# Optimization experiments

Measured on AMD Instinct MI355X. Metric: run time of the kernel, lower is better.

Reference implementation:

```python
import jax, jax.numpy as jnp
import numpy as np

NUM_HEADS = 16
EPS = 1e-5


def _layernorm(x, w):
    # torch LayerNorm (biased variance), bias=False
    m = jnp.mean(x, axis=-1, keepdims=True)
    v = jnp.mean(jnp.square(x - m), axis=-1, keepdims=True)
    return (x - m) * jax.lax.rsqrt(v + EPS) * w


def setup_inputs() -> dict:
    key = jax.random.key(0)
    ks = jax.random.split(key, 8)
    B, S, H, A = 2, 2048, 1024, 1024
    hd = H // NUM_HEADS
    return {
        "x": jax.random.normal(ks[0], (B, S, H), jnp.float32),
        "ada_cond": jax.random.normal(ks[1], (B, A), jnp.float32),
        "freqs": jax.random.normal(ks[2], (S, hd // 2, 2), jnp.float32),
        "w_qkv": jax.random.normal(ks[3], (3 * H, H), jnp.float32) * (1.0 / np.sqrt(H)),
        "w_o": jax.random.normal(ks[4], (H, H), jnp.float32) * (1.0 / np.sqrt(H)),
        "ln_w": jnp.ones((H,), jnp.float32),
        "mod_w": jax.random.normal(ks[5], (3 * H, A), jnp.float32) * 0.02,
        "mod_b": jax.random.normal(ks[6], (3 * H,), jnp.float32) * 0.02,
        "qn_w": jnp.ones((hd,), jnp.float32),
        "kn_w": jnp.ones((hd,), jnp.float32),
    }


def reference(x, ada_cond, freqs, w_qkv, w_o, ln_w, mod_w, mod_b, qn_w, kn_w):
    B, S, H = x.shape
    nh = NUM_HEADS
    hd = H // nh

    # pre-norm + AdaLN modulation (with gate)
    h = _layernorm(x, ln_w)
    mod = (jax.nn.silu(ada_cond) @ mod_w.T + mod_b)[:, None, :]  # [B,1,3H]
    scale, shift, gate = jnp.split(mod, 3, axis=-1)
    h = h * (scale + 1.0) + shift

    # QKV projection and head split
    qkv = h @ w_qkv.T                                  # [B,S,3H]
    q, k, v = jnp.split(qkv, 3, axis=-1)
    to_heads = lambda t: t.reshape(B, S, nh, hd).transpose(0, 2, 1, 3)  # [B,nh,S,hd]
    q, k, v = to_heads(q), to_heads(k), to_heads(v)

    # per-head QK layernorm
    q = _layernorm(q, qn_w)
    k = _layernorm(k, kn_w)

    # RoPE (complex rotation via interleaved pairs)
    f = freqs[:S].reshape(1, 1, S, hd // 2, 2)

    def rope(t):
        tr = t.reshape(B, nh, S, hd // 2, 2)
        re = tr[..., 0] * f[..., 0] - tr[..., 1] * f[..., 1]
        im = tr[..., 1] * f[..., 0] + tr[..., 0] * f[..., 1]
        return jnp.stack([re, im], axis=-1).reshape(B, nh, S, hd)

    q, k = rope(q), rope(k)

    # scaled dot-product attention (non-causal)
    scores = jnp.einsum("bhqd,bhkd->bhqk", q, k) * (1.0 / np.sqrt(hd))
    attn = jax.nn.softmax(scores, axis=-1)
    o = jnp.einsum("bhqk,bhkd->bhqd", attn, v)
    o = o.transpose(0, 2, 1, 3).reshape(B, S, H)

    return (o @ w_o.T) * gate
```

## Files before the change

kernel.cpp:

```cpp
#include <hip/hip_runtime.h>
#include <hip/hip_bf16.h>
#include <hip/hip_fp16.h>
#include <math.h>

#define B_ 2
#define S_ 2048
#define H_ 1024
#define A_ 1024
#define NH_ 16
#define HD_ 64
#define H3_ 3072
#define EPS_ 1e-5f

typedef __attribute__((ext_vector_type(8))) short short8;
typedef __attribute__((ext_vector_type(4))) float floatx4;
typedef __attribute__((ext_vector_type(4))) _Float16 half4v;
typedef __attribute__((ext_vector_type(2))) __fp16 fp16x2;

__device__ inline unsigned short f2bf(float x) {
    union { float f; unsigned u; } v; v.f = x;
    unsigned r = v.u + 0x7fffu + ((v.u >> 16) & 1u);
    return (unsigned short)(r >> 16);
}

__device__ inline unsigned pk_bf16(float a, float b) {
    union { __hip_bfloat162 h; unsigned u; } v;
    v.h = __float22bfloat162_rn(make_float2(a, b));
    return v.u;
}

__device__ inline unsigned pk_f16(float a, float b) {
    union { __half2 h; unsigned u; } v;
    v.h = __float22half2_rn(make_float2(a, b));
    return v.u;
}

__device__ inline void gld_lds16(const void* g, void* l) {
    __builtin_amdgcn_global_load_lds(
        (const __attribute__((address_space(1))) unsigned int*)g,
        (__attribute__((address_space(3))) unsigned int*)l, 16, 0, 0);
}


__global__ __launch_bounds__(256) void cast_bf16_kernel(
    const float* __restrict__ in, unsigned short* __restrict__ out, int n)
{
    int i = (blockIdx.x * 256 + threadIdx.x) * 8;
    if (i >= n) return;
    float4 a = *(const float4*)(in + i);
    float4 b = *(const float4*)(in + i + 4);
    uint4 o;
    o.x = pk_bf16(a.x, a.y);
    o.y = pk_bf16(a.z, a.w);
    o.z = pk_bf16(b.x, b.y);
    o.w = pk_bf16(b.z, b.w);
    *(uint4*)(out + i) = o;
}

__global__ __launch_bounds__(256) void mod_gemv_kernel(
    const float* __restrict__ ada, const float* __restrict__ mod_w,
    const float* __restrict__ mod_b, float* __restrict__ mod)
{
    int wid = threadIdx.x >> 6;
    int lane = threadIdx.x & 63;
    int idx = blockIdx.x * 4 + wid;
    int b = idx / H3_;
    int j = idx % H3_;
    const float* ar = ada + (size_t)b * A_;
    const float* wr = mod_w + (size_t)j * A_;
    float acc = 0.f;
    for (int a = lane; a < A_; a += 64) {
        float av = ar[a];
        float sv = av / (1.f + __expf(-av));
        acc += sv * wr[a];
    }
    #pragma unroll
    for (int m = 1; m < 64; m <<= 1) acc += __shfl_xor(acc, m);
    if (lane == 0) mod[idx] = acc + mod_b[j];
}

__global__ __launch_bounds__(256) void ln_mod_kernel(
    const float* __restrict__ x, const float* __restrict__ ln_w,
    const float* __restrict__ mod, unsigned short* __restrict__ hout)
{
    int row = blockIdx.x;
    int b = row >> 11;
    const float* xr = x + (size_t)row * H_;
    int t = threadIdx.x;
    float4 xv = *(const float4*)(xr + t * 4);
    float s1 = xv.x + xv.y + xv.z + xv.w;
    float s2 = xv.x*xv.x + xv.y*xv.y + xv.z*xv.z + xv.w*xv.w;
    #pragma unroll
    for (int m = 1; m < 64; m <<= 1) { s1 += __shfl_xor(s1, m); s2 += __shfl_xor(s2, m); }
    __shared__ float r1[4], r2[4];
    int wid = t >> 6, lane = t & 63;
    if (lane == 0) { r1[wid] = s1; r2[wid] = s2; }
    __syncthreads();
    s1 = r1[0] + r1[1] + r1[2] + r1[3];
    s2 = r2[0] + r2[1] + r2[2] + r2[3];
    float mean = s1 * (1.f / H_);
    float var  = s2 * (1.f / H_) - mean * mean;
    float rstd = rsqrtf(var + EPS_);
    const float* mrow = mod + (size_t)b * H3_;
    float4 wv = *(const float4*)(ln_w + t * 4);
    float4 sc = *(const float4*)(mrow + t * 4);
    float4 sh = *(const float4*)(mrow + H_ + t * 4);
    float4 hv;
    hv.x = (xv.x - mean) * rstd * wv.x * (sc.x + 1.f) + sh.x;
    hv.y = (xv.y - mean) * rstd * wv.y * (sc.y + 1.f) + sh.y;
    hv.z = (xv.z - mean) * rstd * wv.z * (sc.z + 1.f) + sh.z;
    hv.w = (xv.w - mean) * rstd * wv.w * (sc.w + 1.f) + sh.w;
    uint2 o;
    o.x = pk_bf16(hv.x, hv.y);
    o.y = pk_bf16(hv.z, hv.w);
    *(uint2*)(hout + (size_t)row * H_ + t * 4) = o;
}

__global__ __launch_bounds__(256) void gemm_qkv_fused_kernel(
    const unsigned short* __restrict__ A, const unsigned short* __restrict__ Bm,
    const float* __restrict__ freqs, const float* __restrict__ qn_w,
    const float* __restrict__ kn_w, unsigned short* __restrict__ qout,
    unsigned short* __restrict__ kout, unsigned short* __restrict__ vtout)
{
    __shared__ unsigned short As[2][128 * 32];
    __shared__ unsigned short Bs[2][128 * 32];
    const int K = H_;
    int t = threadIdx.x;
    int w = t >> 6, lane = t & 63;
    int q16 = lane & 15, quad = lane >> 4;
    int wm = w >> 1, wn = w & 1;
    int m0 = blockIdx.y * 128, n0 = blockIdx.x * 128;

    int srow = 2 * (lane >> 3) + ((lane >> 2) & 1);
    int scol = ((lane & 3) ^ ((lane >> 3) & 3)) << 3;
    const unsigned short* ga = A + (size_t)(m0 + (w << 5) + srow) * K + scol;
    const unsigned short* gb = Bm + (size_t)(n0 + (w << 5) + srow) * K + scol;
    int ldst0 = (w * 16) * 64;
    int ldst1 = (w * 16 + 8) * 64;

    floatx4 acc[4][4];
    #pragma unroll
    for (int mt = 0; mt < 4; ++mt)
        #pragma unroll
        for (int nt = 0; nt < 4; ++nt)
            acc[mt][nt] = (floatx4){0.f, 0.f, 0.f, 0.f};

    int abase = (wm * 32 + (q16 >> 1)) * 64 + (q16 & 1) * 32
              + ((quad ^ ((q16 >> 1) & 3)) << 3);
    int bbase = (wn * 32 + (q16 >> 1)) * 64 + (q16 & 1) * 32
              + ((quad ^ ((q16 >> 1) & 3)) << 3);

    gld_lds16(ga, &As[0][ldst0]);
    gld_lds16(ga + (size_t)16 * K, &As[0][ldst1]);
    gld_lds16(gb, &Bs[0][ldst0]);
    gld_lds16(gb + (size_t)16 * K, &Bs[0][ldst1]);
    __syncthreads();

    int cur = 0;
    for (int kt = 0; kt < K / 32; ++kt) {
        const unsigned short* curA = &As[cur][0];
        const unsigned short* curB = &Bs[cur][0];
        short8 af[4], bf[4];
        #pragma unroll
        for (int mt = 0; mt < 4; ++mt)
            af[mt] = *(const short8*)&curA[abase + mt * 512];
        #pragma unroll
        for (int nt = 0; nt < 4; ++nt)
            bf[nt] = *(const short8*)&curB[bbase + nt * 512];

        if (kt + 1 < K / 32) {
            const unsigned short* ga2 = ga + (kt + 1) * 32;
            const unsigned short* gb2 = gb + (kt + 1) * 32;
            int nb = cur ^ 1;
            gld_lds16(ga2, &As[nb][ldst0]);
            gld_lds16(ga2 + (size_t)16 * K, &As[nb][ldst1]);
            gld_lds16(gb2, &Bs[nb][ldst0]);
            gld_lds16(gb2 + (size_t)16 * K, &Bs[nb][ldst1]);
        }

        #pragma unroll
        for (int mt = 0; mt < 4; ++mt)
            #pragma unroll
            for (int nt = 0; nt < 4; ++nt)
                acc[mt][nt] = __builtin_amdgcn_mfma_f32_16x16x32_bf16(
                    af[mt], bf[nt], acc[mt][nt], 0, 0, 0);

        __syncthreads();
        cur ^= 1;
    }

    int n_base = n0 + wn * 64;
    int sec = n_base >> 10;
    int head = (n_base & 1023) >> 6;

    if (sec == 2) {
        #pragma unroll
        for (int mt = 0; mt < 4; ++mt) {
            int m = m0 + wm * 64 + mt * 16 + quad * 4;
            int b = m >> 11, s = m & (S_ - 1);
            #pragma unroll
            for (int nt = 0; nt < 4; ++nt) {
                int d = nt * 16 + q16;
                unsigned short* dst =
                    vtout + ((size_t)((b * 16 + head) * 64 + d)) * S_ + s;
                uint2 pk;
                pk.x = pk_f16(acc[mt][nt][0], acc[mt][nt][1]);
                pk.y = pk_f16(acc[mt][nt][2], acc[mt][nt][3]);
                *(uint2*)dst = pk;
            }
        }
    } else {
        const float* nw = (sec == 0) ? qn_w : kn_w;
        float w4[4];
        #pragma unroll
        for (int nt = 0; nt < 4; ++nt) w4[nt] = nw[nt * 16 + q16];
        unsigned short* outp = (sec == 0) ? qout : kout;
        float qscale = (sec == 0) ? 0.1803368801111244f : 1.0f;

        #pragma unroll
        for (int mt = 0; mt < 4; ++mt) {
            #pragma unroll
            for (int i = 0; i < 4; ++i) {
                int m = m0 + wm * 64 + mt * 16 + quad * 4 + i;
                int b = m >> 11, s = m & (S_ - 1);
                float v0 = acc[mt][0][i], v1 = acc[mt][1][i];
                float v2 = acc[mt][2][i], v3 = acc[mt][3][i];
                float s1 = (v0 + v1) + (v2 + v3);
                float s2 = (v0 * v0 + v1 * v1) + (v2 * v2 + v3 * v3);
                #pragma unroll
                for (int msk = 1; msk < 16; msk <<= 1) {
                    s1 += __shfl_xor(s1, msk);
                    s2 += __shfl_xor(s2, msk);
                }
                float mean = s1 * (1.f / 64);
                float var  = s2 * (1.f / 64) - mean * mean;
                float rstd = rsqrtf(var + EPS_);
                float vv[4];
                vv[0] = (v0 - mean) * rstd * w4[0];
                vv[1] = (v1 - mean) * rstd * w4[1];
                vv[2] = (v2 - mean) * rstd * w4[2];
                vv[3] = (v3 - mean) * rstd * w4[3];
                const float* fr = freqs + (size_t)s * 64;
                unsigned short* orow = outp + ((size_t)((b * 16 + head) * S_ + s)) * 64;
                #pragma unroll
                for (int nt = 0; nt < 4; ++nt) {
                    int c = nt * 16 + q16;
                    float vp = __shfl_xor(vv[nt], 1);
                    float2 ff = *(const float2*)(fr + (c & ~1));
                    float r = (c & 1) ? (vv[nt] * ff.x + vp * ff.y)
                                      : (vv[nt] * ff.x - vp * ff.y);
                    orow[c] = f2bf(r * qscale);
                }
            }
        }
    }
}

__global__ __launch_bounds__(256) void gemm_bt_bf16_kernel(
    const unsigned short* __restrict__ A, const unsigned short* __restrict__ Bm,
    float* __restrict__ C, int M, int N, int K,
    const float* __restrict__ gate, int gate_stride, int batch_shift)
{
    __shared__ unsigned short As[2][128 * 32];
    __shared__ unsigned short Bs[2][128 * 32];
    int t = threadIdx.x;
    int w = t >> 6, lane = t & 63;
    int q16 = lane & 15, quad = lane >> 4;
    int wm = w >> 1, wn = w & 1;
    int m0 = blockIdx.y * 128, n0 = blockIdx.x * 128;

    int srow = 2 * (lane >> 3) + ((lane >> 2) & 1);
    int scol = ((lane & 3) ^ ((lane >> 3) & 3)) << 3;
    const unsigned short* ga = A + (size_t)(m0 + (w << 5) + srow) * K + scol;
    const unsigned short* gb = Bm + (size_t)(n0 + (w << 5) + srow) * K + scol;
    int ldst0 = (w * 16) * 64;
    int ldst1 = (w * 16 + 8) * 64;

    floatx4 acc[4][4];
    #pragma unroll
    for (int mt = 0; mt < 4; ++mt)
        #pragma unroll
        for (int nt = 0; nt < 4; ++nt)
            acc[mt][nt] = (floatx4){0.f, 0.f, 0.f, 0.f};

    int abase = (wm * 32 + (q16 >> 1)) * 64 + (q16 & 1) * 32
              + ((quad ^ ((q16 >> 1) & 3)) << 3);
    int bbase = (wn * 32 + (q16 >> 1)) * 64 + (q16 & 1) * 32
              + ((quad ^ ((q16 >> 1) & 3)) << 3);

    gld_lds16(ga, &As[0][ldst0]);
    gld_lds16(ga + (size_t)16 * K, &As[0][ldst1]);
    gld_lds16(gb, &Bs[0][ldst0]);
    gld_lds16(gb + (size_t)16 * K, &Bs[0][ldst1]);
    __syncthreads();

    int cur = 0;
    for (int kt = 0; kt < K / 32; ++kt) {
        const unsigned short* curA = &As[cur][0];
        const unsigned short* curB = &Bs[cur][0];
        short8 af[4], bf[4];
        #pragma unroll
        for (int mt = 0; mt < 4; ++mt)
            af[mt] = *(const short8*)&curA[abase + mt * 512];
        #pragma unroll
        for (int nt = 0; nt < 4; ++nt)
            bf[nt] = *(const short8*)&curB[bbase + nt * 512];

        if (kt + 1 < K / 32) {
            const unsigned short* ga2 = ga + (kt + 1) * 32;
            const unsigned short* gb2 = gb + (kt + 1) * 32;
            int nb = cur ^ 1;
            gld_lds16(ga2, &As[nb][ldst0]);
            gld_lds16(ga2 + (size_t)16 * K, &As[nb][ldst1]);
            gld_lds16(gb2, &Bs[nb][ldst0]);
            gld_lds16(gb2 + (size_t)16 * K, &Bs[nb][ldst1]);
        }

        #pragma unroll
        for (int mt = 0; mt < 4; ++mt)
            #pragma unroll
            for (int nt = 0; nt < 4; ++nt)
                acc[mt][nt] = __builtin_amdgcn_mfma_f32_16x16x32_bf16(
                    af[mt], bf[nt], acc[mt][nt], 0, 0, 0);

        __syncthreads();
        cur ^= 1;
    }

    #pragma unroll
    for (int mt = 0; mt < 4; ++mt) {
        #pragma unroll
        for (int i = 0; i < 4; ++i) {
            int m = m0 + wm * 64 + mt * 16 + quad * 4 + i;
            float* crow = C + (size_t)m * N;
            const float* grow = gate ? gate + (size_t)(m >> batch_shift) * gate_stride
                                     : nullptr;
            #pragma unroll
            for (int nt = 0; nt < 4; ++nt) {
                int n = n0 + wn * 64 + nt * 16 + q16;
                float v = acc[mt][nt][i];
                if (gate) v *= grow[n];
                crow[n] = v;
            }
        }
    }
}

__global__ __launch_bounds__(256, 2) void attn_mfma_kernel(
    const unsigned short* __restrict__ q, const unsigned short* __restrict__ k,
    const unsigned short* __restrict__ vt, unsigned short* __restrict__ o)
{
    __shared__ __align__(16) unsigned char smem[16 * 1024];
    __shared__ float lbuf[4][4][16];
    unsigned short* Vs = (unsigned short*)smem;

    int t = threadIdx.x;
    int w = t >> 6, lane = t & 63;
    int q16 = lane & 15, quad = lane >> 4;
    int bh = blockIdx.y, b = bh >> 4, h = bh & 15;
    int s0 = blockIdx.x * 64;

    const unsigned short* qgp = q + ((size_t)bh * S_ + s0) * HD_;
    short8 qf[4][2];
    #pragma unroll
    for (int qg = 0; qg < 4; ++qg)
        #pragma unroll
        for (int hh = 0; hh < 2; ++hh)
            qf[qg][hh] = *(const short8*)(qgp + (16 * qg + q16) * HD_ + hh * 32 + quad * 8);

    const unsigned short* kg = k + (size_t)bh * S_ * HD_ + (16 * w + q16) * HD_ + quad * 8;

    const unsigned short* vg0 = vt + (size_t)bh * 64 * S_
                              + (size_t)(16 * w + (lane >> 3)) * S_ + (lane & 7) * 8;
    const unsigned short* vg1 = vg0 + 8 * S_;
    unsigned short* vw0 = Vs + (16 * w + (lane >> 3)) * 64 + (((lane & 7) ^ (lane >> 3)) << 3);
    unsigned short* vw1 = vw0 + 512;
    int vroff = q16 * 64 + (((2 * w + (quad >> 1)) ^ (q16 & 7)) << 3) + ((quad & 1) << 2);

    short8 kf_nx0 = *(const short8*)kg;
    short8 kf_nx1 = *(const short8*)(kg + 32);
    uint4 vr0 = *(const uint4*)vg0;
    uint4 vr1 = *(const uint4*)vg1;

    union { half4v h; uint2 u; } ones;
    ones.u.x = 0x3C003C00u; ones.u.y = 0x3C003C00u;

    floatx4 acc_o[4][4];
    floatx4 acc_l[4];
    #pragma unroll
    for (int nd = 0; nd < 4; ++nd)
        #pragma unroll
        for (int qg = 0; qg < 4; ++qg)
            acc_o[nd][qg] = (floatx4){0.f, 0.f, 0.f, 0.f};
    #pragma unroll
    for (int qg = 0; qg < 4; ++qg) acc_l[qg] = (floatx4){0.f, 0.f, 0.f, 0.f};

    for (int kt = 0; kt < S_ / 64; ++kt) {
        short8 kf0 = kf_nx0, kf1 = kf_nx1;
        uint4 v0 = vr0, v1 = vr1;
        __syncthreads();
        *(uint4*)vw0 = v0;
        *(uint4*)vw1 = v1;
        __syncthreads();

        if (kt + 1 < S_ / 64) {
            kg += 64 * HD_; vg0 += 64; vg1 += 64;
            kf_nx0 = *(const short8*)kg;
            kf_nx1 = *(const short8*)(kg + 32);
            vr0 = *(const uint4*)vg0;
            vr1 = *(const uint4*)vg1;
        }

        floatx4 sc[4];
        #pragma unroll
        for (int qg = 0; qg < 4; ++qg) sc[qg] = (floatx4){-12.f, -12.f, -12.f, -12.f};
        #pragma unroll
        for (int qg = 0; qg < 4; ++qg) {
            sc[qg] = __builtin_amdgcn_mfma_f32_16x16x32_bf16(kf0, qf[qg][0], sc[qg], 0, 0, 0);
            sc[qg] = __builtin_amdgcn_mfma_f32_16x16x32_bf16(kf1, qf[qg][1], sc[qg], 0, 0, 0);
        }

        half4v vf[4];
        #pragma unroll
        for (int nd = 0; nd < 4; ++nd)
            vf[nd] = *(const half4v*)&Vs[vroff + nd * 1024];

        #pragma unroll
        for (int qg = 0; qg < 4; ++qg) {
            float p0 = __builtin_amdgcn_exp2f(sc[qg][0]);
            float p1 = __builtin_amdgcn_exp2f(sc[qg][1]);
            float p2 = __builtin_amdgcn_exp2f(sc[qg][2]);
            float p3 = __builtin_amdgcn_exp2f(sc[qg][3]);
            union { half4v h; fp16x2 f2[2]; } pf;
            pf.f2[0] = __builtin_amdgcn_cvt_pkrtz(p0, p1);
            pf.f2[1] = __builtin_amdgcn_cvt_pkrtz(p2, p3);
            acc_l[qg] = __builtin_amdgcn_mfma_f32_16x16x16f16(ones.h, pf.h, acc_l[qg], 0, 0, 0);
            #pragma unroll
            for (int nd = 0; nd < 4; ++nd)
                acc_o[nd][qg] = __builtin_amdgcn_mfma_f32_16x16x16f16(
                    vf[nd], pf.h, acc_o[nd][qg], 0, 0, 0);
        }
    }

    if (quad == 0) {
        #pragma unroll
        for (int qg = 0; qg < 4; ++qg) lbuf[w][qg][q16] = acc_l[qg][0];
    }
    __syncthreads();
    float linv = 1.f / (lbuf[0][w][q16] + lbuf[1][w][q16] + lbuf[2][w][q16] + lbuf[3][w][q16]);

    float* obuf = (float*)smem;
    float* myw = obuf + ((w * 4) * 64 + lane) * 4;
    float* myr = obuf + (w * 64 + lane) * 4;
    unsigned short* og = o + ((size_t)(b * S_ + s0 + 16 * w + q16)) * H_ + h * HD_ + 4 * quad;

    #pragma unroll
    for (int nd = 0; nd < 4; ++nd) {
        __syncthreads();
        #pragma unroll
        for (int qg = 0; qg < 4; ++qg)
            *(floatx4*)(myw + qg * 256) = acc_o[nd][qg];
        __syncthreads();
        floatx4 r0 = *(const floatx4*)(myr);
        floatx4 r1 = *(const floatx4*)(myr + 1024);
        floatx4 r2 = *(const floatx4*)(myr + 2048);
        floatx4 r3 = *(const floatx4*)(myr + 3072);
        floatx4 s = (r0 + r1) + (r2 + r3);
        uint2 pk;
        pk.x = pk_bf16(s[0] * linv, s[1] * linv);
        pk.y = pk_bf16(s[2] * linv, s[3] * linv);
        *(uint2*)(og + nd * 16) = pk;
    }
}

extern "C" void kernel_launch(void* const* d_in, const int* in_sizes, int n_in,
                              void* d_out, int out_size, void* d_ws, size_t ws_size,
                              hipStream_t stream)
{
    const float* x     = (const float*)d_in[0];
    const float* ada   = (const float*)d_in[1];
    const float* freqs = (const float*)d_in[2];
    const float* w_qkv = (const float*)d_in[3];
    const float* w_o   = (const float*)d_in[4];
    const float* ln_w  = (const float*)d_in[5];
    const float* mod_w = (const float*)d_in[6];
    const float* mod_b = (const float*)d_in[7];
    const float* qn_w  = (const float*)d_in[8];
    const float* kn_w  = (const float*)d_in[9];
    float* out = (float*)d_out;

    float* ws  = (float*)d_ws;
    float* mod = ws;
    unsigned short* hb    = (unsigned short*)(mod + 8192);
    unsigned short* qb    = hb + (size_t)B_ * S_ * H_;
    unsigned short* kb    = qb + (size_t)B_ * S_ * H_;
    unsigned short* vtb   = kb + (size_t)B_ * S_ * H_;
    unsigned short* ob    = vtb + (size_t)B_ * S_ * H_;
    unsigned short* wqkvb = ob + (size_t)B_ * S_ * H_;
    unsigned short* wob   = wqkvb + (size_t)H3_ * H_;

    cast_bf16_kernel<<<H3_ * H_ / (8 * 256), 256, 0, stream>>>(w_qkv, wqkvb, H3_ * H_);
    cast_bf16_kernel<<<H_ * H_ / (8 * 256), 256, 0, stream>>>(w_o, wob, H_ * H_);
    mod_gemv_kernel<<<B_ * H3_ / 4, 256, 0, stream>>>(ada, mod_w, mod_b, mod);
    ln_mod_kernel<<<B_ * S_, 256, 0, stream>>>(x, ln_w, mod, hb);
    gemm_qkv_fused_kernel<<<dim3(H3_ / 128, B_ * S_ / 128), 256, 0, stream>>>(
        hb, wqkvb, freqs, qn_w, kn_w, qb, kb, vtb);
    attn_mfma_kernel<<<dim3(S_ / 64, B_ * NH_), 256, 0, stream>>>(qb, kb, vtb, ob);
    gemm_bt_bf16_kernel<<<dim3(H_ / 128, B_ * S_ / 128), 256, 0, stream>>>(
        ob, wob, out, B_ * S_, H_, H_, mod + 2 * H_, H3_, 11);
}
```

Measured before the change: 263.6 us.

## Load V fragments directly from global in attention; shrink output GEMM tile to 128x64

The attention kernel stops staging V through LDS with two barriers per key tile. Each lane now loads its V fragments straight from global memory into registers and prefetches the next tile's fragments. This removes the per-iteration syncthreads and LDS traffic, at the cost of smaller, less coalesced global reads and more registers. The output-projection GEMM also moves from 128x128 to 128x64 tiles, doubling the block count from 256 to 512 to fill more CUs, but with less operand reuse per block.

```diff
diff --git a/kernel.cpp b/kernel.cpp
--- a/kernel.cpp
+++ b/kernel.cpp
@@ -262,45 +262,44 @@
     const float* __restrict__ gate, int gate_stride, int batch_shift)
 {
     __shared__ unsigned short As[2][128 * 32];
-    __shared__ unsigned short Bs[2][128 * 32];
+    __shared__ unsigned short Bs[2][64 * 32];
     int t = threadIdx.x;
     int w = t >> 6, lane = t & 63;
     int q16 = lane & 15, quad = lane >> 4;
-    int wm = w >> 1, wn = w & 1;
-    int m0 = blockIdx.y * 128, n0 = blockIdx.x * 128;
+    int m0 = blockIdx.y * 128, n0 = blockIdx.x * 64;
 
     int srow = 2 * (lane >> 3) + ((lane >> 2) & 1);
     int scol = ((lane & 3) ^ ((lane >> 3) & 3)) << 3;
     const unsigned short* ga = A + (size_t)(m0 + (w << 5) + srow) * K + scol;
-    const unsigned short* gb = Bm + (size_t)(n0 + (w << 5) + srow) * K + scol;
-    int ldst0 = (w * 16) * 64;
-    int ldst1 = (w * 16 + 8) * 64;
-
-    floatx4 acc[4][4];
-    #pragma unroll
-    for (int mt = 0; mt < 4; ++mt)
+    const unsigned short* gb = Bm + (size_t)(n0 + (w << 4) + srow) * K + scol;
+    int ldstA0 = (w * 16) * 64;
+    int ldstA1 = (w * 16 + 8) * 64;
+    int ldstB  = (w * 8) * 64;
+
+    floatx4 acc[2][4];
+    #pragma unroll
+    for (int mt = 0; mt < 2; ++mt)
         #pragma unroll
         for (int nt = 0; nt < 4; ++nt)
             acc[mt][nt] = (floatx4){0.f, 0.f, 0.f, 0.f};
 
-    int abase = (wm * 32 + (q16 >> 1)) * 64 + (q16 & 1) * 32
+    int abase = (w * 16 + (q16 >> 1)) * 64 + (q16 & 1) * 32
               + ((quad ^ ((q16 >> 1) & 3)) << 3);
-    int bbase = (wn * 32 + (q16 >> 1)) * 64 + (q16 & 1) * 32
+    int bbase = (q16 >> 1) * 64 + (q16 & 1) * 32
               + ((quad ^ ((q16 >> 1) & 3)) << 3);
 
-    gld_lds16(ga, &As[0][ldst0]);
-    gld_lds16(ga + (size_t)16 * K, &As[0][ldst1]);
-    gld_lds16(gb, &Bs[0][ldst0]);
-    gld_lds16(gb + (size_t)16 * K, &Bs[0][ldst1]);
+    gld_lds16(ga, &As[0][ldstA0]);
+    gld_lds16(ga + (size_t)16 * K, &As[0][ldstA1]);
+    gld_lds16(gb, &Bs[0][ldstB]);
     __syncthreads();
 
     int cur = 0;
     for (int kt = 0; kt < K / 32; ++kt) {
         const unsigned short* curA = &As[cur][0];
         const unsigned short* curB = &Bs[cur][0];
-        short8 af[4], bf[4];
-        #pragma unroll
-        for (int mt = 0; mt < 4; ++mt)
+        short8 af[2], bf[4];
+        #pragma unroll
+        for (int mt = 0; mt < 2; ++mt)
             af[mt] = *(const short8*)&curA[abase + mt * 512];
         #pragma unroll
         for (int nt = 0; nt < 4; ++nt)
@@ -310,14 +309,13 @@
             const unsigned short* ga2 = ga + (kt + 1) * 32;
             const unsigned short* gb2 = gb + (kt + 1) * 32;
             int nb = cur ^ 1;
-            gld_lds16(ga2, &As[nb][ldst0]);
-            gld_lds16(ga2 + (size_t)16 * K, &As[nb][ldst1]);
-            gld_lds16(gb2, &Bs[nb][ldst0]);
-            gld_lds16(gb2 + (size_t)16 * K, &Bs[nb][ldst1]);
-        }
-
-        #pragma unroll
-        for (int mt = 0; mt < 4; ++mt)
+            gld_lds16(ga2, &As[nb][ldstA0]);
+            gld_lds16(ga2 + (size_t)16 * K, &As[nb][ldstA1]);
+            gld_lds16(gb2, &Bs[nb][ldstB]);
+        }
+
+        #pragma unroll
+        for (int mt = 0; mt < 2; ++mt)
             #pragma unroll
             for (int nt = 0; nt < 4; ++nt)
                 acc[mt][nt] = __builtin_amdgcn_mfma_f32_16x16x32_bf16(
@@ -328,16 +326,16 @@
     }
 
     #pragma unroll
-    for (int mt = 0; mt < 4; ++mt) {
+    for (int mt = 0; mt < 2; ++mt) {
         #pragma unroll
         for (int i = 0; i < 4; ++i) {
-            int m = m0 + wm * 64 + mt * 16 + quad * 4 + i;
+            int m = m0 + w * 32 + mt * 16 + quad * 4 + i;
             float* crow = C + (size_t)m * N;
             const float* grow = gate ? gate + (size_t)(m >> batch_shift) * gate_stride
                                      : nullptr;
             #pragma unroll
             for (int nt = 0; nt < 4; ++nt) {
-                int n = n0 + wn * 64 + nt * 16 + q16;
+                int n = n0 + nt * 16 + q16;
                 float v = acc[mt][nt][i];
                 if (gate) v *= grow[n];
                 crow[n] = v;
@@ -350,9 +348,8 @@
     const unsigned short* __restrict__ q, const unsigned short* __restrict__ k,
     const unsigned short* __restrict__ vt, unsigned short* __restrict__ o)
 {
-    __shared__ __align__(16) unsigned char smem[16 * 1024];
+    __shared__ __align__(16) float obuf[4096];
     __shared__ float lbuf[4][4][16];
-    unsigned short* Vs = (unsigned short*)smem;
 
     int t = threadIdx.x;
     int w = t >> 6, lane = t & 63;
@@ -369,18 +366,15 @@
             qf[qg][hh] = *(const short8*)(qgp + (16 * qg + q16) * HD_ + hh * 32 + quad * 8);
 
     const unsigned short* kg = k + (size_t)bh * S_ * HD_ + (16 * w + q16) * HD_ + quad * 8;
-
-    const unsigned short* vg0 = vt + (size_t)bh * 64 * S_
-                              + (size_t)(16 * w + (lane >> 3)) * S_ + (lane & 7) * 8;
-    const unsigned short* vg1 = vg0 + 8 * S_;
-    unsigned short* vw0 = Vs + (16 * w + (lane >> 3)) * 64 + (((lane & 7) ^ (lane >> 3)) << 3);
-    unsigned short* vw1 = vw0 + 512;
-    int vroff = q16 * 64 + (((2 * w + (quad >> 1)) ^ (q16 & 7)) << 3) + ((quad & 1) << 2);
+    const unsigned short* vg = vt + (size_t)bh * 64 * S_ + (size_t)q16 * S_
+                             + 16 * w + quad * 4;
 
     short8 kf_nx0 = *(const short8*)kg;
     short8 kf_nx1 = *(const short8*)(kg + 32);
-    uint4 vr0 = *(const uint4*)vg0;
-    uint4 vr1 = *(const uint4*)vg1;
+    half4v vf_nx[4];
+    #pragma unroll
+    for (int nd = 0; nd < 4; ++nd)
+        vf_nx[nd] = *(const half4v*)(vg + nd * 16 * S_);
 
     union { half4v h; uint2 u; } ones;
     ones.u.x = 0x3C003C00u; ones.u.y = 0x3C003C00u;
@@ -397,18 +391,15 @@
 
     for (int kt = 0; kt < S_ / 64; ++kt) {
         short8 kf0 = kf_nx0, kf1 = kf_nx1;
-        uint4 v0 = vr0, v1 = vr1;
-        __syncthreads();
-        *(uint4*)vw0 = v0;
-        *(uint4*)vw1 = v1;
-        __syncthreads();
+        half4v vf0 = vf_nx[0], vf1 = vf_nx[1], vf2 = vf_nx[2], vf3 = vf_nx[3];
 
         if (kt + 1 < S_ / 64) {
-            kg += 64 * HD_; vg0 += 64; vg1 += 64;
+            kg += 64 * HD_; vg += 64;
             kf_nx0 = *(const short8*)kg;
             kf_nx1 = *(const short8*)(kg + 32);
-            vr0 = *(const uint4*)vg0;
-            vr1 = *(const uint4*)vg1;
+            #pragma unroll
+            for (int nd = 0; nd < 4; ++nd)
+                vf_nx[nd] = *(const half4v*)(vg + nd * 16 * S_);
         }
 
         floatx4 sc[4];
@@ -419,11 +410,6 @@
             sc[qg] = __builtin_amdgcn_mfma_f32_16x16x32_bf16(kf0, qf[qg][0], sc[qg], 0, 0, 0);
             sc[qg] = __builtin_amdgcn_mfma_f32_16x16x32_bf16(kf1, qf[qg][1], sc[qg], 0, 0, 0);
         }
-
-        half4v vf[4];
-        #pragma unroll
-        for (int nd = 0; nd < 4; ++nd)
-            vf[nd] = *(const half4v*)&Vs[vroff + nd * 1024];
 
         #pragma unroll
         for (int qg = 0; qg < 4; ++qg) {
@@ -435,10 +421,10 @@
             pf.f2[0] = __builtin_amdgcn_cvt_pkrtz(p0, p1);
             pf.f2[1] = __builtin_amdgcn_cvt_pkrtz(p2, p3);
             acc_l[qg] = __builtin_amdgcn_mfma_f32_16x16x16f16(ones.h, pf.h, acc_l[qg], 0, 0, 0);
-            #pragma unroll
-            for (int nd = 0; nd < 4; ++nd)
-                acc_o[nd][qg] = __builtin_amdgcn_mfma_f32_16x16x16f16(
-                    vf[nd], pf.h, acc_o[nd][qg], 0, 0, 0);
+            acc_o[0][qg] = __builtin_amdgcn_mfma_f32_16x16x16f16(vf0, pf.h, acc_o[0][qg], 0, 0, 0);
+            acc_o[1][qg] = __builtin_amdgcn_mfma_f32_16x16x16f16(vf1, pf.h, acc_o[1][qg], 0, 0, 0);
+            acc_o[2][qg] = __builtin_amdgcn_mfma_f32_16x16x16f16(vf2, pf.h, acc_o[2][qg], 0, 0, 0);
+            acc_o[3][qg] = __builtin_amdgcn_mfma_f32_16x16x16f16(vf3, pf.h, acc_o[3][qg], 0, 0, 0);
         }
     }
 
@@ -449,7 +435,6 @@
     __syncthreads();
     float linv = 1.f / (lbuf[0][w][q16] + lbuf[1][w][q16] + lbuf[2][w][q16] + lbuf[3][w][q16]);
 
-    float* obuf = (float*)smem;
     float* myw = obuf + ((w * 4) * 64 + lane) * 4;
     float* myr = obuf + (w * 64 + lane) * 4;
     unsigned short* og = o + ((size_t)(b * S_ + s0 + 16 * w + q16)) * H_ + h * HD_ + 4 * quad;
@@ -506,6 +491,6 @@
     gemm_qkv_fused_kernel<<<dim3(H3_ / 128, B_ * S_ / 128), 256, 0, stream>>>(
         hb, wqkvb, freqs, qn_w, kn_w, qb, kb, vtb);
     attn_mfma_kernel<<<dim3(S_ / 64, B_ * NH_), 256, 0, stream>>>(qb, kb, vtb, ob);
-    gemm_bt_bf16_kernel<<<dim3(H_ / 128, B_ * S_ / 128), 256, 0, stream>>>(
+    gemm_bt_bf16_kernel<<<dim3(H_ / 64, B_ * S_ / 128), 256, 0, stream>>>(
         ob, wob, out, B_ * S_, H_, H_, mod + 2 * H_, H3_, 11);
 }
```

After: 286.2 us. 8.6% more time.
